# Performance work log

Measured on AMD Instinct MI355X. Metric: run time of the kernel, lower is better.

## Reference

```python
import jax, jax.numpy as jnp
import numpy as np
from jax import lax

THRESH = 0.8
LENS = 0.4
DECAY = 0.2
LOG_SIG_MIN, LOG_SIG_MAX = -20.0, 2.0
WINS = 15

@jax.custom_vjp
def act_fun(x):
    return (x > THRESH).astype(x.dtype)

def _act_fwd(x):
    return act_fun(x), x

def _act_bwd(x, g):
    return (g * (jnp.abs(x - THRESH) < LENS).astype(g.dtype),)

act_fun.defvjp(_act_fwd, _act_bwd)

B, NIN, HID, NACT = 2048, 512, 1024, 32

def _xavier(key, out_d, in_d):
    lim = jnp.sqrt(6.0 / (in_d + out_d)).astype(jnp.float32)
    return jax.random.uniform(key, (out_d, in_d), jnp.float32, -lim, lim)

def setup_inputs() -> dict:
    key = jax.random.key(0)
    ks = jax.random.split(key, 12)
    inp = {
        'state': jax.random.normal(ks[0], (B, 5, NIN), jnp.float32),
        'w1': _xavier(ks[1], HID, NIN), 'b1': jnp.zeros((HID,), jnp.float32),
        'w2': _xavier(ks[2], HID, NIN), 'b2': jnp.zeros((HID,), jnp.float32),
        'w3': _xavier(ks[3], HID, NIN), 'b3': jnp.zeros((HID,), jnp.float32),
        'wl': _xavier(ks[4], 1, 3), 'bl': jnp.zeros((1,), jnp.float32),
        'w11': _xavier(ks[5], HID, 4 * HID), 'b11': jnp.zeros((HID,), jnp.float32),
        'w12': _xavier(ks[6], HID, HID), 'b12': jnp.zeros((HID,), jnp.float32),
        'w21': _xavier(ks[7], HID, 4 * HID), 'b21': jnp.zeros((HID,), jnp.float32),
        'w22': _xavier(ks[8], HID, HID), 'b22': jnp.zeros((HID,), jnp.float32),
        'wm': _xavier(ks[9], NACT, HID), 'bm': jnp.zeros((NACT,), jnp.float32),
        'ws': _xavier(ks[10], NACT, HID), 'bs': jnp.zeros((NACT,), jnp.float32),
    }
    return inp

def _policy_forward(state, w1, b1, w2, b2, w3, b3, wl, bl,
                    w11, b11, w12, b12, w21, b21, w22, b22, wm, bm, ws, bs):
    batch = state.shape[0]
    hid = w1.shape[0]
    seq = jnp.repeat(state, 3, axis=1)
    mem0 = jnp.zeros((batch, hid, 4), state.dtype)
    sp0 = jnp.zeros((batch, hid, 4), state.dtype)

    def step(carry, x_t):
        mem, spike = carry
        i1 = x_t @ w1.T + b1  # [B, HID]
        i2 = x_t @ w2.T + b2
        i3 = x_t @ w3.T + b3
        inner = jnp.einsum('bck,k->bc', mem[:, :, :3], wl[0]) + bl[0]
        inp_all = jnp.stack([i1, i2, i3, inner], axis=-1)  # [B, HID, 4]
        mem1 = mem * DECAY * (1.0 - spike) + inp_all
        sp1 = act_fun(mem1)
        return (mem1, sp1), sp1

    _, spikes = lax.scan(step, (mem0, sp0), jnp.swapaxes(seq, 0, 1))  # [T,B,HID,4]
    spikes = jnp.transpose(spikes, (1, 0, 2, 3)).reshape(batch, WINS, hid * 4)
    x = jnp.mean(spikes, axis=1)  # [B, 4*HID]

    x1 = jax.nn.relu(x @ w11.T + b11)
    x1 = jax.nn.relu(x1 @ w12.T + b12)
    mean = x1 @ wm.T + bm

    x2 = jax.nn.relu(x @ w21.T + b21)
    x2 = jax.nn.relu(x2 @ w22.T + b22)
    log_std = jnp.clip(x2 @ ws.T + bs, LOG_SIG_MIN, LOG_SIG_MAX)
    return mean, log_std

def reference(state, w1, b1, w2, b2, w3, b3, wl, bl,
              w11, b11, w12, b12, w21, b21, w22, b22, wm, bm, ws, bs):
    return _policy_forward(state, w1, b1, w2, b2, w3, b3, wl, bl,
                           w11, b11, w12, b12, w21, b21, w22, b22, wm, bm, ws, bs)
```

## Files before the change

### kernel.cpp

```cpp
#include <hip/hip_runtime.h>
#include <cstddef>
#include <cstdint>

#define THRESH 0.8f
#define DECAY  0.2f

typedef unsigned short ushort_t;
typedef __attribute__((ext_vector_type(8))) short bf16x8;
typedef __attribute__((ext_vector_type(4))) float f32x4;
typedef __attribute__((ext_vector_type(4))) int i32x4;

__device__ __forceinline__ ushort_t f2bf(float f) {
    union { float f; unsigned u; } v; v.f = f;
    unsigned r = v.u + 0x7FFFu + ((v.u >> 16) & 1u);
    return (ushort_t)(r >> 16);
}
__device__ __forceinline__ float bf2f(ushort_t h) {
    union { unsigned u; float f; } v; v.u = ((unsigned)h) << 16;
    return v.f;
}
__device__ __forceinline__ float blo(unsigned u) {
    union { unsigned x; float f; } v; v.x = u << 16; return v.f;
}
__device__ __forceinline__ float bhi(unsigned u) {
    union { unsigned x; float f; } v; v.x = u & 0xFFFF0000u; return v.f;
}

__device__ __forceinline__ void gload16(const void* g, void* l) {
    __builtin_amdgcn_global_load_lds(
        (const __attribute__((address_space(1))) void*)g,
        (__attribute__((address_space(3))) void*)l,
        16, 0, 0);
}

__global__ __launch_bounds__(512, 2) void cur_gemm_qb(
    const ushort_t* __restrict__ A, const ushort_t* __restrict__ W,
    const float* __restrict__ bias, float* __restrict__ C)
{
    __shared__ ushort_t lds[4][16384];

    const int t = threadIdx.x;
    const int mBase = blockIdx.x * 256;
    const int nBase = blockIdx.y * 256;

    const int lane = t & 63;
    const int wv = t >> 6;
    const int wm = (wv >> 2) * 128;
    const int wn = (wv & 3) * 64;
    const int fr = lane & 15;
    const int fq = lane >> 4;
    const int fsw = (fq ^ ((fr >> 1) & 3)) * 8;

    const int r0 = t >> 2;
    const int sc0 = ((t & 3) ^ ((r0 >> 1) & 3)) * 8;
    const size_t aRow0 = (size_t)(mBase + r0) * 1536 + sc0;
    const size_t aRow1 = (size_t)(mBase + r0 + 128) * 1536 + sc0;
    const size_t wRow0 = (size_t)(nBase + r0) * 1536 + sc0;
    const size_t wRow1 = (size_t)(nBase + r0 + 128) * 1536 + sc0;

    f32x4 acc[8][4];
#pragma unroll
    for (int i = 0; i < 8; i++)
#pragma unroll
        for (int j = 0; j < 4; j++) {
            f32x4 z = {0.f, 0.f, 0.f, 0.f};
            acc[i][j] = z;
        }

#define STAGE(tile)                                                   \
    do {                                                              \
        const int k0_ = (tile) * 32;                                  \
        ushort_t* lb_ = &lds[(tile) & 3][0];                          \
        gload16(&A[aRow0 + k0_], &lb_[t * 8]);                        \
        gload16(&A[aRow1 + k0_], &lb_[4096 + t * 8]);                 \
        gload16(&W[wRow0 + k0_], &lb_[8192 + t * 8]);                 \
        gload16(&W[wRow1 + k0_], &lb_[12288 + t * 8]);                \
    } while (0)

    STAGE(0);
    STAGE(1);

    for (int tt = 0; tt < 48; ++tt) {
        if (tt < 47) {
            asm volatile("s_waitcnt vmcnt(4)" ::: "memory");
        } else {
            asm volatile("s_waitcnt vmcnt(0)" ::: "memory");
        }
        __builtin_amdgcn_s_barrier();
        __builtin_amdgcn_sched_barrier(0);
        if (tt < 46) STAGE(tt + 2);

        const ushort_t* lb = &lds[tt & 3][0];
        bf16x8 af[8], wf[4];
#pragma unroll
        for (int i = 0; i < 8; i++)
            af[i] = *(const bf16x8*)&lb[(wm + i * 16 + fr) * 32 + fsw];
#pragma unroll
        for (int j = 0; j < 4; j++)
            wf[j] = *(const bf16x8*)&lb[8192 + (wn + j * 16 + fr) * 32 + fsw];

        __builtin_amdgcn_s_setprio(1);
#pragma unroll
        for (int i = 0; i < 8; i++)
#pragma unroll
            for (int j = 0; j < 4; j++)
                acc[i][j] = __builtin_amdgcn_mfma_f32_16x16x32_bf16(af[i], wf[j], acc[i][j], 0, 0, 0);
        __builtin_amdgcn_s_setprio(0);
    }
#undef STAGE

#pragma unroll
    for (int j = 0; j < 4; j++) {
        const int col = nBase + wn + j * 16 + fr;
        const float bv = bias[col];
#pragma unroll
        for (int i = 0; i < 8; i++)
#pragma unroll
            for (int r = 0; r < 4; r++) {
                const int row = mBase + wm + i * 16 + fq * 4 + r;
                C[(size_t)row * 3072 + col] = acc[i][j][r] + bv;
            }
    }
}

__global__ __launch_bounds__(256) void mlp1_i8(
    const signed char* __restrict__ A, const signed char* __restrict__ W,
    const float* __restrict__ wsc, const float* __restrict__ bias,
    ushort_t* __restrict__ C)
{
    __shared__ signed char sA[64 * 64];
    __shared__ signed char sW[128 * 64];

    const int t = threadIdx.x;
    const int mBase = blockIdx.x * 64;
    const int nBase = blockIdx.y * 128;

    const int lane = t & 63;
    const int wv = t >> 6;
    const int wn = wv * 32;
    const int fr = lane & 15;
    const int fq = lane >> 4;
    const int fsw = (fq ^ ((fr >> 1) & 3)) * 16;

    const int r0 = t >> 2;
    const int cc = ((t & 3) ^ ((t >> 3) & 3)) * 16;

    i32x4 acc[4][2];
#pragma unroll
    for (int i = 0; i < 4; i++)
#pragma unroll
        for (int j = 0; j < 2; j++) {
            i32x4 z = {0, 0, 0, 0};
            acc[i][j] = z;
        }

    for (int k0 = 0; k0 < 4096; k0 += 64) {
        gload16(&A[(size_t)(mBase + r0) * 4096 + k0 + cc], &sA[t * 16]);
        gload16(&W[(size_t)(nBase + r0) * 4096 + k0 + cc], &sW[t * 16]);
        gload16(&W[(size_t)(nBase + 64 + r0) * 4096 + k0 + cc], &sW[4096 + t * 16]);
        __syncthreads();

        i32x4 af[4], wf[2];
#pragma unroll
        for (int i = 0; i < 4; i++)
            af[i] = *(const i32x4*)&sA[(i * 16 + fr) * 64 + fsw];
#pragma unroll
        for (int j = 0; j < 2; j++)
            wf[j] = *(const i32x4*)&sW[(wn + j * 16 + fr) * 64 + fsw];
#pragma unroll
        for (int i = 0; i < 4; i++)
#pragma unroll
            for (int j = 0; j < 2; j++)
                acc[i][j] = __builtin_amdgcn_mfma_i32_16x16x64_i8(af[i], wf[j], acc[i][j], 0, 0, 0);
        __syncthreads();
    }

#pragma unroll
    for (int j = 0; j < 2; j++) {
        const int col = nBase + wn + j * 16 + fr;
        const float sc = wsc[col];
        const float bv = bias[col];
#pragma unroll
        for (int i = 0; i < 4; i++)
#pragma unroll
            for (int r = 0; r < 4; r++) {
                const int row = mBase + i * 16 + fq * 4 + r;
                const float v = (float)acc[i][j][r] * sc + bv;
                C[(size_t)row * 2048 + col] = f2bf(fmaxf(v, 0.f));
            }
    }
}

__global__ __launch_bounds__(256) void mlp2_bf16(
    const ushort_t* __restrict__ A, const ushort_t* __restrict__ W,
    const float* __restrict__ bias, ushort_t* __restrict__ C,
    int N, int K, int lda, int ldw, int ldc, int aHalfOff)
{
    __shared__ ushort_t sA[64 * 32];
    __shared__ ushort_t sW[128 * 32];

    const int t = threadIdx.x;
    const int mBase = blockIdx.x * 64;
    const int nBase = blockIdx.y * 128;
    const int aOff = (2 * nBase >= N) ? aHalfOff : 0;

    const int lane = t & 63;
    const int wv = t >> 6;
    const int wn = wv * 32;
    const int fr = lane & 15;
    const int fq = lane >> 4;
    const int fsw = (fq ^ ((fr >> 1) & 3)) * 8;

    const int r0 = t >> 2;
    const int cc = ((t & 3) ^ ((t >> 3) & 3)) * 8;

    f32x4 acc[4][2];
#pragma unroll
    for (int i = 0; i < 4; i++)
#pragma unroll
        for (int j = 0; j < 2; j++) {
            f32x4 z = {0.f, 0.f, 0.f, 0.f};
            acc[i][j] = z;
        }

    for (int k0 = 0; k0 < K; k0 += 32) {
        gload16(&A[(size_t)(mBase + r0) * lda + aOff + k0 + cc], &sA[t * 8]);
        gload16(&W[(size_t)(nBase + r0) * ldw + k0 + cc], &sW[t * 8]);
        gload16(&W[(size_t)(nBase + 64 + r0) * ldw + k0 + cc], &sW[2048 + t * 8]);
        __syncthreads();

        bf16x8 af[4], wf[2];
#pragma unroll
        for (int i = 0; i < 4; i++)
            af[i] = *(const bf16x8*)&sA[(i * 16 + fr) * 32 + fsw];
#pragma unroll
        for (int j = 0; j < 2; j++)
            wf[j] = *(const bf16x8*)&sW[(wn + j * 16 + fr) * 32 + fsw];
#pragma unroll
        for (int i = 0; i < 4; i++)
#pragma unroll
            for (int j = 0; j < 2; j++)
                acc[i][j] = __builtin_amdgcn_mfma_f32_16x16x32_bf16(af[i], wf[j], acc[i][j], 0, 0, 0);
        __syncthreads();
    }

#pragma unroll
    for (int j = 0; j < 2; j++) {
        const int col = nBase + wn + j * 16 + fr;
        const float bv = bias[col];
#pragma unroll
        for (int i = 0; i < 4; i++)
#pragma unroll
            for (int r = 0; r < 4; r++) {
                const int row = mBase + i * 16 + fq * 4 + r;
                C[(size_t)row * ldc + col] = f2bf(fmaxf(acc[i][j][r] + bv, 0.f));
            }
    }
}

__global__ __launch_bounds__(256) void recur_kernel(
    const float* __restrict__ cur, const float* __restrict__ wl,
    const float* __restrict__ bl, signed char* __restrict__ x)
{
    const int idx = blockIdx.x * 256 + threadIdx.x;
    const int b = idx >> 10, c = idx & 1023;
    const float wl0 = wl[0], wl1 = wl[1], wl2 = wl[2], bl0 = bl[0];
    float m0 = 0, m1 = 0, m2 = 0, m3 = 0;
    int s0 = 0, s1 = 0, s2 = 0, s3 = 0;
#pragma unroll
    for (int f = 0; f < 5; f++) {
        const float* p = cur + (size_t)(b * 5 + f) * 3072 + c;
        const float i1 = p[0], i2 = p[1024], i3 = p[2048];
#pragma unroll
        for (int rep = 0; rep < 3; rep++) {
            const float inner = m0 * wl0 + m1 * wl1 + m2 * wl2 + bl0;
            const float n0 = i1 + ((m0 > THRESH) ? 0.f : DECAY * m0);
            const float n1 = i2 + ((m1 > THRESH) ? 0.f : DECAY * m1);
            const float n2 = i3 + ((m2 > THRESH) ? 0.f : DECAY * m2);
            const float n3 = inner + ((m3 > THRESH) ? 0.f : DECAY * m3);
            m0 = n0; m1 = n1; m2 = n2; m3 = n3;
            s0 += (n0 > THRESH); s1 += (n1 > THRESH);
            s2 += (n2 > THRESH); s3 += (n3 > THRESH);
        }
    }
    uchar4 o;
    o.x = (unsigned char)s0; o.y = (unsigned char)s1;
    o.z = (unsigned char)s2; o.w = (unsigned char)s3;
    *(uchar4*)&x[(size_t)b * 4096 + c * 4] = o;
}

__device__ __forceinline__ void split_state(const float4* src, ushort4* dst,
                                            int base, int t) {
#pragma unroll
    for (int p = 0; p < 4; p++) {
        const int i = base * 1024 + p * 256 + t;
        const float4 v = src[i];
        ushort4 h, l;
        h.x = f2bf(v.x); l.x = f2bf(v.x - bf2f(h.x));
        h.y = f2bf(v.y); l.y = f2bf(v.y - bf2f(h.y));
        h.z = f2bf(v.z); l.z = f2bf(v.z - bf2f(h.z));
        h.w = f2bf(v.w); l.w = f2bf(v.w - bf2f(h.w));
        const int r = i >> 7, c = i & 127;
        ushort4* row = dst + (size_t)r * 384;
        row[c] = h; row[128 + c] = h; row[256 + c] = l;
    }
}
__device__ __forceinline__ void split_w(const float4* src, ushort4* dst,
                                        int base, int t, int roff) {
#pragma unroll
    for (int p = 0; p < 4; p++) {
        const int i = base * 1024 + p * 256 + t;
        const float4 v = src[i];
        ushort4 h, l;
        h.x = f2bf(v.x); l.x = f2bf(v.x - bf2f(h.x));
        h.y = f2bf(v.y); l.y = f2bf(v.y - bf2f(h.y));
        h.z = f2bf(v.z); l.z = f2bf(v.z - bf2f(h.z));
        h.w = f2bf(v.w); l.w = f2bf(v.w - bf2f(h.w));
        const int r = (i >> 7) + roff, c = i & 127;
        ushort4* row = dst + (size_t)r * 384;
        row[c] = h; row[128 + c] = l; row[256 + c] = h;
    }
}
__device__ __forceinline__ void do_cvt4(const float4* src, ushort4* dst,
                                        int base, int t) {
#pragma unroll
    for (int p = 0; p < 4; p++) {
        const int i = base * 1024 + p * 256 + t;
        const float4 v = src[i];
        ushort4 h;
        h.x = f2bf(v.x); h.y = f2bf(v.y); h.z = f2bf(v.z); h.w = f2bf(v.w);
        dst[i] = h;
    }
}
__device__ __forceinline__ int q8(float x, float inv) {
    int q = (int)rintf(x * inv);
    q = q > 127 ? 127 : (q < -127 ? -127 : q);
    return q & 0xff;
}

__global__ __launch_bounds__(256) void prep_kernel(
    const float* __restrict__ state,
    const float* __restrict__ w1, const float* __restrict__ w2,
    const float* __restrict__ w3,
    const float* __restrict__ w11, const float* __restrict__ w21,
    const float* __restrict__ w12, const float* __restrict__ w22,
    const float* __restrict__ b1, const float* __restrict__ b2,
    const float* __restrict__ b3, const float* __restrict__ b11,
    const float* __restrict__ b21, const float* __restrict__ b12,
    const float* __restrict__ b22,
    ushort_t* __restrict__ Ap, ushort_t* __restrict__ Wp,
    signed char* __restrict__ w1q, float* __restrict__ wsc,
    ushort_t* __restrict__ w2b,
    float* __restrict__ b123, float* __restrict__ bb1, float* __restrict__ bb2)
{
    const int bid = blockIdx.x;
    const int t = threadIdx.x;
    if (bid < 1280) {
        split_state((const float4*)state, (ushort4*)Ap, bid, t);
    } else if (bid < 1408) {
        split_w((const float4*)w1, (ushort4*)Wp, bid - 1280, t, 0);
    } else if (bid < 1536) {
        split_w((const float4*)w2, (ushort4*)Wp, bid - 1408, t, 1024);
    } else if (bid < 1664) {
        split_w((const float4*)w3, (ushort4*)Wp, bid - 1536, t, 2048);
    } else if (bid < 3712) {
        const int r = bid - 1664;
        const float* src = (r < 1024) ? (w11 + (size_t)r * 4096)
                                      : (w21 + (size_t)(r - 1024) * 4096);
        __shared__ float red[256];
        float4 v[4];
        float lmax = 0.f;
#pragma unroll
        for (int p = 0; p < 4; p++) {
            v[p] = ((const float4*)src)[t * 4 + p];
            lmax = fmaxf(lmax, fmaxf(fmaxf(fabsf(v[p].x), fabsf(v[p].y)),
                                     fmaxf(fabsf(v[p].z), fabsf(v[p].w))));
        }
        red[t] = lmax;
        __syncthreads();
        for (int s = 128; s > 0; s >>= 1) {
            if (t < s) red[t] = fmaxf(red[t], red[t + s]);
            __syncthreads();
        }
        const float gmax = fmaxf(red[0], 1e-30f);
        const float inv = 127.0f / gmax;
        int4 o;
        o.x = q8(v[0].x, inv) | (q8(v[0].y, inv) << 8) | (q8(v[0].z, inv) << 16) | (q8(v[0].w, inv) << 24);
        o.y = q8(v[1].x, inv) | (q8(v[1].y, inv) << 8) | (q8(v[1].z, inv) << 16) | (q8(v[1].w, inv) << 24);
        o.z = q8(v[2].x, inv) | (q8(v[2].y, inv) << 8) | (q8(v[2].z, inv) << 16) | (q8(v[2].w, inv) << 24);
        o.w = q8(v[3].x, inv) | (q8(v[3].y, inv) << 8) | (q8(v[3].z, inv) << 16) | (q8(v[3].w, inv) << 24);
        ((int4*)(w1q + (size_t)r * 4096))[t] = o;
        if (t == 0) wsc[r] = gmax / (127.0f * 15.0f);
    } else if (bid < 3968) {
        do_cvt4((const float4*)w12, (ushort4*)w2b, bid - 3712, t);
    } else if (bid < 4224) {
        do_cvt4((const float4*)w22, (ushort4*)(w2b + 1048576), bid - 3968, t);
    } else {
#pragma unroll
        for (int p = 0; p < 4; p++) {
            const int i = p * 256 + t;
            b123[i] = b1[i]; b123[1024 + i] = b2[i]; b123[2048 + i] = b3[i];
            bb1[i] = b11[i]; bb1[1024 + i] = b21[i];
            bb2[i] = b12[i]; bb2[1024 + i] = b22[i];
        }
    }
}

__global__ __launch_bounds__(256) void head_kernel(
    const ushort_t* __restrict__ h, const float* __restrict__ wm,
    const float* __restrict__ bm, const float* __restrict__ ws,
    const float* __restrict__ bs, float* __restrict__ out)
{
    const int t = threadIdx.x;
    const int branch = blockIdx.x >> 8;
    const int n = t & 31;
    const int b = (blockIdx.x & 255) * 8 + (t >> 5);
    const ushort_t* hr = h + (size_t)b * 2048 + branch * 1024;
    const float* wr = (branch ? ws : wm) + (size_t)n * 1024;
    float s = 0.f;
#pragma unroll 4
    for (int k = 0; k < 1024; k += 8) {
        const uint4 hv = *(const uint4*)&hr[k];
        const float4 w0 = *(const float4*)&wr[k];
        const float4 w1 = *(const float4*)&wr[k + 4];
        s += blo(hv.x) * w0.x + bhi(hv.x) * w0.y
           + blo(hv.y) * w0.z + bhi(hv.y) * w0.w
           + blo(hv.z) * w1.x + bhi(hv.z) * w1.y
           + blo(hv.w) * w1.z + bhi(hv.w) * w1.w;
    }
    s += (branch ? bs : bm)[n];
    if (branch) s = fminf(fmaxf(s, -20.f), 2.f);
    out[(size_t)branch * 65536 + (size_t)b * 32 + n] = s;
}

extern "C" void kernel_launch(void* const* d_in, const int* in_sizes, int n_in,
                              void* d_out, int out_size, void* d_ws, size_t ws_size,
                              hipStream_t stream)
{
    const float* state = (const float*)d_in[0];
    const float* w1  = (const float*)d_in[1];  const float* b1  = (const float*)d_in[2];
    const float* w2  = (const float*)d_in[3];  const float* b2  = (const float*)d_in[4];
    const float* w3  = (const float*)d_in[5];  const float* b3  = (const float*)d_in[6];
    const float* wl  = (const float*)d_in[7];  const float* bl  = (const float*)d_in[8];
    const float* w11 = (const float*)d_in[9];  const float* b11 = (const float*)d_in[10];
    const float* w12 = (const float*)d_in[11]; const float* b12 = (const float*)d_in[12];
    const float* w21 = (const float*)d_in[13]; const float* b21 = (const float*)d_in[14];
    const float* w22 = (const float*)d_in[15]; const float* b22 = (const float*)d_in[16];
    const float* wm  = (const float*)d_in[17]; const float* bm  = (const float*)d_in[18];
    const float* ws  = (const float*)d_in[19]; const float* bs  = (const float*)d_in[20];
    float* out = (float*)d_out;

    char* wp = (char*)d_ws;
    float*       cur   = (float*)wp;       wp += (size_t)10240 * 3072 * 4;
    ushort_t*    Ap    = (ushort_t*)wp;    wp += (size_t)10240 * 1536 * 2;
    ushort_t*    Wp    = (ushort_t*)wp;    wp += (size_t)3072 * 1536 * 2;
    signed char* xb    = (signed char*)wp; wp += (size_t)2048 * 4096;
    signed char* w1q   = (signed char*)wp; wp += (size_t)2048 * 4096;
    ushort_t*    w2b   = (ushort_t*)wp;    wp += (size_t)2048 * 1024 * 2;
    ushort_t*    h1    = (ushort_t*)wp;    wp += (size_t)2048 * 2048 * 2;
    ushort_t*    h2    = (ushort_t*)wp;    wp += (size_t)2048 * 2048 * 2;
    float*       wsc   = (float*)wp;       wp += 2048 * 4;
    float*       b123  = (float*)wp;       wp += 3072 * 4;
    float*       bb1   = (float*)wp;       wp += 2048 * 4;
    float*       bb2   = (float*)wp;       wp += 2048 * 4;

    prep_kernel<<<4225, 256, 0, stream>>>(
        state, w1, w2, w3, w11, w21, w12, w22,
        b1, b2, b3, b11, b21, b12, b22,
        Ap, Wp, w1q, wsc, w2b, b123, bb1, bb2);

    cur_gemm_qb<<<dim3(40, 12), 512, 0, stream>>>(Ap, Wp, b123, cur);

    recur_kernel<<<8192, 256, 0, stream>>>(cur, wl, bl, xb);

    mlp1_i8<<<dim3(32, 16), 256, 0, stream>>>(xb, w1q, wsc, bb1, h1);

    mlp2_bf16<<<dim3(32, 16), 256, 0, stream>>>(
        h1, w2b, bb2, h2, 2048, 1024, 2048, 1024, 2048, 1024);

    head_kernel<<<512, 256, 0, stream>>>(h2, wm, bm, ws, bs, out);
}
```

Measured before the change: 379.1 us.

## Split GEMM k-step into two phases interleaving LDS reads, global prefetch and MFMA

Result: no change. 386.5 us (+1.9%).

```diff
diff --git a/kernel.cpp b/kernel.cpp
--- a/kernel.cpp
+++ b/kernel.cpp
@@ -33,7 +33,13 @@
         16, 0, 0);
 }
 
-__global__ __launch_bounds__(512, 2) void cur_gemm_qb(
+#define DSREAD(dst, addr, off) \
+    asm volatile("ds_read_b128 %0, %1 offset:" #off : "=v"(dst) : "v"(addr))
+
+#define MM(i, j, a, w) \
+    acc[i][j] = __builtin_amdgcn_mfma_f32_16x16x32_bf16(a, w, acc[i][j], 0, 0, 0)
+
+__global__ __launch_bounds__(512, 2) void cur_gemm_8ph(
     const ushort_t* __restrict__ A, const ushort_t* __restrict__ W,
     const float* __restrict__ bias, float* __restrict__ C)
 {
@@ -49,7 +55,10 @@
     const int wn = (wv & 3) * 64;
     const int fr = lane & 15;
     const int fq = lane >> 4;
-    const int fsw = (fq ^ ((fr >> 1) & 3)) * 8;
+    const int fsw2 = (fq ^ ((fr >> 1) & 3)) * 16;
+
+    const unsigned aBase = (unsigned)((wm + fr) * 64 + fsw2);
+    const unsigned bBase = (unsigned)(16384 + (wn + fr) * 64 + fsw2);
 
     const int r0 = t >> 2;
     const int sc0 = ((t & 3) ^ ((r0 >> 1) & 3)) * 8;
@@ -67,47 +76,67 @@
             acc[i][j] = z;
         }
 
-#define STAGE(tile)                                                   \
-    do {                                                              \
-        const int k0_ = (tile) * 32;                                  \
-        ushort_t* lb_ = &lds[(tile) & 3][0];                          \
-        gload16(&A[aRow0 + k0_], &lb_[t * 8]);                        \
-        gload16(&A[aRow1 + k0_], &lb_[4096 + t * 8]);                 \
-        gload16(&W[wRow0 + k0_], &lb_[8192 + t * 8]);                 \
-        gload16(&W[wRow1 + k0_], &lb_[12288 + t * 8]);                \
-    } while (0)
-
-    STAGE(0);
-    STAGE(1);
+#define STG_A0(tile) gload16(&A[aRow0 + (size_t)(tile) * 32], &lds[(tile) & 3][t * 8])
+#define STG_A1(tile) gload16(&A[aRow1 + (size_t)(tile) * 32], &lds[(tile) & 3][4096 + t * 8])
+#define STG_B0(tile) gload16(&W[wRow0 + (size_t)(tile) * 32], &lds[(tile) & 3][8192 + t * 8])
+#define STG_B1(tile) gload16(&W[wRow1 + (size_t)(tile) * 32], &lds[(tile) & 3][12288 + t * 8])
+
+    STG_A0(0); STG_A1(0); STG_B0(0); STG_B1(0);
+    STG_A0(1); STG_A1(1); STG_B0(1); STG_B1(1);
+    asm volatile("s_waitcnt vmcnt(4)");
+    __builtin_amdgcn_s_barrier();
 
     for (int tt = 0; tt < 48; ++tt) {
-        if (tt < 47) {
-            asm volatile("s_waitcnt vmcnt(4)" ::: "memory");
-        } else {
-            asm volatile("s_waitcnt vmcnt(0)" ::: "memory");
-        }
+        const unsigned bufOff = (unsigned)((tt & 3) << 15);
+        const unsigned av = aBase + bufOff;
+        const unsigned bv = bBase + bufOff;
+        bf16x8 af0, af1, af2, af3, wf0, wf1, wf2, wf3;
+
+        DSREAD(af0, av, 0);
+        DSREAD(af1, av, 1024);
+        DSREAD(af2, av, 2048);
+        DSREAD(af3, av, 3072);
+        DSREAD(wf0, bv, 0);
+        DSREAD(wf1, bv, 1024);
+        DSREAD(wf2, bv, 2048);
+        DSREAD(wf3, bv, 3072);
+        if (tt < 46) { STG_A0(tt + 2); STG_A1(tt + 2); }
         __builtin_amdgcn_s_barrier();
+        asm volatile("s_waitcnt lgkmcnt(0)");
         __builtin_amdgcn_sched_barrier(0);
-        if (tt < 46) STAGE(tt + 2);
-
-        const ushort_t* lb = &lds[tt & 3][0];
-        bf16x8 af[8], wf[4];
-#pragma unroll
-        for (int i = 0; i < 8; i++)
-            af[i] = *(const bf16x8*)&lb[(wm + i * 16 + fr) * 32 + fsw];
-#pragma unroll
-        for (int j = 0; j < 4; j++)
-            wf[j] = *(const bf16x8*)&lb[8192 + (wn + j * 16 + fr) * 32 + fsw];
-
         __builtin_amdgcn_s_setprio(1);
-#pragma unroll
-        for (int i = 0; i < 8; i++)
-#pragma unroll
-            for (int j = 0; j < 4; j++)
-                acc[i][j] = __builtin_amdgcn_mfma_f32_16x16x32_bf16(af[i], wf[j], acc[i][j], 0, 0, 0);
+        MM(0, 0, af0, wf0); MM(0, 1, af0, wf1); MM(0, 2, af0, wf2); MM(0, 3, af0, wf3);
+        MM(1, 0, af1, wf0); MM(1, 1, af1, wf1); MM(1, 2, af1, wf2); MM(1, 3, af1, wf3);
+        MM(2, 0, af2, wf0); MM(2, 1, af2, wf1); MM(2, 2, af2, wf2); MM(2, 3, af2, wf3);
+        MM(3, 0, af3, wf0); MM(3, 1, af3, wf1); MM(3, 2, af3, wf2); MM(3, 3, af3, wf3);
         __builtin_amdgcn_s_setprio(0);
-    }
-#undef STAGE
+        __builtin_amdgcn_s_barrier();
+
+        DSREAD(af0, av, 4096);
+        DSREAD(af1, av, 5120);
+        DSREAD(af2, av, 6144);
+        DSREAD(af3, av, 7168);
+        if (tt < 46) { STG_B0(tt + 2); STG_B1(tt + 2); }
+        if (tt < 46) {
+            asm volatile("s_waitcnt vmcnt(4)");
+        } else if (tt == 46) {
+            asm volatile("s_waitcnt vmcnt(0)");
+        }
+        __builtin_amdgcn_s_barrier();
+        asm volatile("s_waitcnt lgkmcnt(0)");
+        __builtin_amdgcn_sched_barrier(0);
+        __builtin_amdgcn_s_setprio(1);
+        MM(4, 0, af0, wf0); MM(4, 1, af0, wf1); MM(4, 2, af0, wf2); MM(4, 3, af0, wf3);
+        MM(5, 0, af1, wf0); MM(5, 1, af1, wf1); MM(5, 2, af1, wf2); MM(5, 3, af1, wf3);
+        MM(6, 0, af2, wf0); MM(6, 1, af2, wf1); MM(6, 2, af2, wf2); MM(6, 3, af2, wf3);
+        MM(7, 0, af3, wf0); MM(7, 1, af3, wf1); MM(7, 2, af3, wf2); MM(7, 3, af3, wf3);
+        __builtin_amdgcn_s_setprio(0);
+        __builtin_amdgcn_s_barrier();
+    }
+#undef STG_A0
+#undef STG_A1
+#undef STG_B0
+#undef STG_B1
 
 #pragma unroll
     for (int j = 0; j < 4; j++) {
@@ -469,7 +498,7 @@
         b1, b2, b3, b11, b21, b12, b22,
         Ap, Wp, w1q, wsc, w2b, b123, bb1, bb2);
 
-    cur_gemm_qb<<<dim3(40, 12), 512, 0, stream>>>(Ap, Wp, b123, cur);
+    cur_gemm_8ph<<<dim3(40, 12), 512, 0, stream>>>(Ap, Wp, b123, cur);
 
     recur_kernel<<<8192, 256, 0, stream>>>(cur, wl, bl, xb);
 
```

## Fuse input-current GEMM with LIF recurrence via permuted operand layouts

Applied to the files above, without the earlier changes.

New measurement: 370.1 us. 2.4% less time.

```diff
diff --git a/kernel.cpp b/kernel.cpp
--- a/kernel.cpp
+++ b/kernel.cpp
@@ -33,93 +33,158 @@
         16, 0, 0);
 }
 
-__global__ __launch_bounds__(512, 2) void cur_gemm_qb(
+#define DSREAD(dst, addr, off) \
+    asm volatile("ds_read_b128 %0, %1 offset:" #off : "=v"(dst) : "v"(addr))
+
+#define MM(i, j, a, w) \
+    acc[i][j] = __builtin_amdgcn_mfma_f32_16x16x32_bf16(a, w, acc[i][j], 0, 0, 0)
+
+__global__ __launch_bounds__(512, 4) void fused_cur_lif(
     const ushort_t* __restrict__ A, const ushort_t* __restrict__ W,
-    const float* __restrict__ bias, float* __restrict__ C)
+    const float* __restrict__ b123, const float* __restrict__ wl,
+    const float* __restrict__ bl, signed char* __restrict__ xb)
 {
-    __shared__ ushort_t lds[4][16384];
+    __shared__ ushort_t lds[3][11264];
 
     const int t = threadIdx.x;
-    const int mBase = blockIdx.x * 256;
-    const int nBase = blockIdx.y * 256;
-
+    const int bx = blockIdx.x;
+    const int by = blockIdx.y;
     const int lane = t & 63;
     const int wv = t >> 6;
-    const int wm = (wv >> 2) * 128;
-    const int wn = (wv & 3) * 64;
+    const int wm = (wv >> 2) * 80;
+    const int wn = (wv & 3) * 48;
     const int fr = lane & 15;
     const int fq = lane >> 4;
-    const int fsw = (fq ^ ((fr >> 1) & 3)) * 8;
-
-    const int r0 = t >> 2;
-    const int sc0 = ((t & 3) ^ ((r0 >> 1) & 3)) * 8;
-    const size_t aRow0 = (size_t)(mBase + r0) * 1536 + sc0;
-    const size_t aRow1 = (size_t)(mBase + r0 + 128) * 1536 + sc0;
-    const size_t wRow0 = (size_t)(nBase + r0) * 1536 + sc0;
-    const size_t wRow1 = (size_t)(nBase + r0 + 128) * 1536 + sc0;
-
-    f32x4 acc[8][4];
-#pragma unroll
-    for (int i = 0; i < 8; i++)
-#pragma unroll
-        for (int j = 0; j < 4; j++) {
+    const int swz16 = (fq ^ ((fr >> 1) & 3)) * 16;
+
+    const unsigned a0 = (unsigned)((wm + fr) * 64 + swz16);
+    const unsigned b0 = (unsigned)(10240 + (wn + fr) * 64 + swz16);
+
+    const ushort_t* src0; const ushort_t* src1;
+    const ushort_t* src2; const ushort_t* src3;
+    int dst0, dst1, dst2, dst3;
+    if (wv < 5) {
+        const int rl0 = wv * 32 + (lane >> 2);
+        const int rl1 = rl0 + 16;
+        src0 = A + (size_t)(bx * 160 + rl0) * 1536 + ((lane & 3) ^ ((rl0 >> 1) & 3)) * 8;
+        src1 = A + (size_t)(bx * 160 + rl1) * 1536 + ((lane & 3) ^ ((rl1 >> 1) & 3)) * 8;
+        src2 = src0; src3 = src1;
+        dst0 = rl0 * 32 + (lane & 3) * 8;
+        dst1 = rl1 * 32 + (lane & 3) * 8;
+        dst2 = dst0; dst3 = dst1;
+    } else {
+        const int rb = (wv - 5) * 64 + (lane >> 2);
+        src0 = W + (size_t)(by * 192 + rb) * 1536 + ((lane & 3) ^ ((rb >> 1) & 3)) * 8;
+        src1 = src0 + (size_t)16 * 1536;
+        src2 = src0 + (size_t)32 * 1536;
+        src3 = src0 + (size_t)48 * 1536;
+        dst0 = 5120 + rb * 32 + (lane & 3) * 8;
+        dst1 = dst0 + 16 * 32;
+        dst2 = dst0 + 32 * 32;
+        dst3 = dst0 + 48 * 32;
+    }
+
+#define STAGE(tile, sbuf)                                              \
+    do {                                                               \
+        const int k0_ = (tile) * 32;                                   \
+        ushort_t* lb_ = &lds[sbuf][0];                                 \
+        if (wv < 5) {                                                  \
+            gload16(src0 + k0_, lb_ + dst0);                           \
+            gload16(src1 + k0_, lb_ + dst1);                           \
+        } else {                                                       \
+            gload16(src0 + k0_, lb_ + dst0);                           \
+            gload16(src1 + k0_, lb_ + dst1);                           \
+            gload16(src2 + k0_, lb_ + dst2);                           \
+            gload16(src3 + k0_, lb_ + dst3);                           \
+        }                                                              \
+    } while (0)
+
+    f32x4 acc[5][3];
+#pragma unroll
+    for (int i = 0; i < 5; i++)
+#pragma unroll
+        for (int j = 0; j < 3; j++) {
             f32x4 z = {0.f, 0.f, 0.f, 0.f};
             acc[i][j] = z;
         }
 
-#define STAGE(tile)                                                   \
-    do {                                                              \
-        const int k0_ = (tile) * 32;                                  \
-        ushort_t* lb_ = &lds[(tile) & 3][0];                          \
-        gload16(&A[aRow0 + k0_], &lb_[t * 8]);                        \
-        gload16(&A[aRow1 + k0_], &lb_[4096 + t * 8]);                 \
-        gload16(&W[wRow0 + k0_], &lb_[8192 + t * 8]);                 \
-        gload16(&W[wRow1 + k0_], &lb_[12288 + t * 8]);                \
-    } while (0)
-
-    STAGE(0);
-    STAGE(1);
-
+    STAGE(0, 0);
+    STAGE(1, 1);
+
+    int cb = 0, sb = 2;
     for (int tt = 0; tt < 48; ++tt) {
-        if (tt < 47) {
-            asm volatile("s_waitcnt vmcnt(4)" ::: "memory");
+        if (tt < 46) STAGE(tt + 2, sb);
+        if (wv < 5) {
+            if (tt < 46)       asm volatile("s_waitcnt vmcnt(4)" ::: "memory");
+            else if (tt == 46) asm volatile("s_waitcnt vmcnt(2)" ::: "memory");
+            else               asm volatile("s_waitcnt vmcnt(0)" ::: "memory");
         } else {
-            asm volatile("s_waitcnt vmcnt(0)" ::: "memory");
+            if (tt < 46)       asm volatile("s_waitcnt vmcnt(8)" ::: "memory");
+            else if (tt == 46) asm volatile("s_waitcnt vmcnt(4)" ::: "memory");
+            else               asm volatile("s_waitcnt vmcnt(0)" ::: "memory");
         }
         __builtin_amdgcn_s_barrier();
         __builtin_amdgcn_sched_barrier(0);
-        if (tt < 46) STAGE(tt + 2);
-
-        const ushort_t* lb = &lds[tt & 3][0];
-        bf16x8 af[8], wf[4];
-#pragma unroll
-        for (int i = 0; i < 8; i++)
-            af[i] = *(const bf16x8*)&lb[(wm + i * 16 + fr) * 32 + fsw];
-#pragma unroll
-        for (int j = 0; j < 4; j++)
-            wf[j] = *(const bf16x8*)&lb[8192 + (wn + j * 16 + fr) * 32 + fsw];
-
+
+        const unsigned av = (unsigned)(cb * 22528) + a0;
+        const unsigned bv = (unsigned)(cb * 22528) + b0;
+        bf16x8 af0, af1, af2, af3, af4, wf0, wf1, wf2;
+        DSREAD(af0, av, 0);
+        DSREAD(af1, av, 1024);
+        DSREAD(af2, av, 2048);
+        DSREAD(af3, av, 3072);
+        DSREAD(af4, av, 4096);
+        DSREAD(wf0, bv, 0);
+        DSREAD(wf1, bv, 1024);
+        DSREAD(wf2, bv, 2048);
+        asm volatile("s_waitcnt lgkmcnt(0)" ::: "memory");
+        __builtin_amdgcn_sched_barrier(0);
         __builtin_amdgcn_s_setprio(1);
-#pragma unroll
-        for (int i = 0; i < 8; i++)
-#pragma unroll
-            for (int j = 0; j < 4; j++)
-                acc[i][j] = __builtin_amdgcn_mfma_f32_16x16x32_bf16(af[i], wf[j], acc[i][j], 0, 0, 0);
+        MM(0, 0, af0, wf0); MM(0, 1, af0, wf1); MM(0, 2, af0, wf2);
+        MM(1, 0, af1, wf0); MM(1, 1, af1, wf1); MM(1, 2, af1, wf2);
+        MM(2, 0, af2, wf0); MM(2, 1, af2, wf1); MM(2, 2, af2, wf2);
+        MM(3, 0, af3, wf0); MM(3, 1, af3, wf1); MM(3, 2, af3, wf2);
+        MM(4, 0, af4, wf0); MM(4, 1, af4, wf1); MM(4, 2, af4, wf2);
         __builtin_amdgcn_s_setprio(0);
+        __builtin_amdgcn_s_barrier();
+        __builtin_amdgcn_sched_barrier(0);
+
+        cb = (cb == 2) ? 0 : cb + 1;
+        sb = (sb == 2) ? 0 : sb + 1;
     }
 #undef STAGE
 
-#pragma unroll
-    for (int j = 0; j < 4; j++) {
-        const int col = nBase + wn + j * 16 + fr;
-        const float bv = bias[col];
-#pragma unroll
-        for (int i = 0; i < 8; i++)
-#pragma unroll
-            for (int r = 0; r < 4; r++) {
-                const int row = mBase + wm + i * 16 + fq * 4 + r;
-                C[(size_t)row * 3072 + col] = acc[i][j][r] + bv;
+    const int ch = by * 64 + (wv & 3) * 16 + fr;
+    const float b1c = b123[ch];
+    const float b2c = b123[1024 + ch];
+    const float b3c = b123[2048 + ch];
+    const float wl0 = wl[0], wl1 = wl[1], wl2 = wl[2], bl0 = bl[0];
+    const int bbase = bx * 32 + (wv >> 2) * 16 + fq * 4;
+#pragma unroll
+    for (int r = 0; r < 4; r++) {
+        float m0 = 0.f, m1 = 0.f, m2 = 0.f, m3 = 0.f;
+        int s0 = 0, s1 = 0, s2 = 0, s3 = 0;
+#pragma unroll
+        for (int f = 0; f < 5; f++) {
+            const float i1 = acc[f][0][r] + b1c;
+            const float i2 = acc[f][1][r] + b2c;
+            const float i3 = acc[f][2][r] + b3c;
+#pragma unroll
+            for (int rep = 0; rep < 3; rep++) {
+                const float inner = m0 * wl0 + m1 * wl1 + m2 * wl2 + bl0;
+                const float n0 = i1 + ((m0 > THRESH) ? 0.f : DECAY * m0);
+                const float n1 = i2 + ((m1 > THRESH) ? 0.f : DECAY * m1);
+                const float n2 = i3 + ((m2 > THRESH) ? 0.f : DECAY * m2);
+                const float n3 = inner + ((m3 > THRESH) ? 0.f : DECAY * m3);
+                m0 = n0; m1 = n1; m2 = n2; m3 = n3;
+                s0 += (n0 > THRESH); s1 += (n1 > THRESH);
+                s2 += (n2 > THRESH); s3 += (n3 > THRESH);
             }
+        }
+        uchar4 o;
+        o.x = (unsigned char)s0; o.y = (unsigned char)s1;
+        o.z = (unsigned char)s2; o.w = (unsigned char)s3;
+        *(uchar4*)&xb[(size_t)(bbase + r) * 4096 + ch * 4] = o;
     }
 }
 
@@ -258,39 +323,8 @@
     }
 }
 
-__global__ __launch_bounds__(256) void recur_kernel(
-    const float* __restrict__ cur, const float* __restrict__ wl,
-    const float* __restrict__ bl, signed char* __restrict__ x)
-{
-    const int idx = blockIdx.x * 256 + threadIdx.x;
-    const int b = idx >> 10, c = idx & 1023;
-    const float wl0 = wl[0], wl1 = wl[1], wl2 = wl[2], bl0 = bl[0];
-    float m0 = 0, m1 = 0, m2 = 0, m3 = 0;
-    int s0 = 0, s1 = 0, s2 = 0, s3 = 0;
-#pragma unroll
-    for (int f = 0; f < 5; f++) {
-        const float* p = cur + (size_t)(b * 5 + f) * 3072 + c;
-        const float i1 = p[0], i2 = p[1024], i3 = p[2048];
-#pragma unroll
-        for (int rep = 0; rep < 3; rep++) {
-            const float inner = m0 * wl0 + m1 * wl1 + m2 * wl2 + bl0;
-            const float n0 = i1 + ((m0 > THRESH) ? 0.f : DECAY * m0);
-            const float n1 = i2 + ((m1 > THRESH) ? 0.f : DECAY * m1);
-            const float n2 = i3 + ((m2 > THRESH) ? 0.f : DECAY * m2);
-            const float n3 = inner + ((m3 > THRESH) ? 0.f : DECAY * m3);
-            m0 = n0; m1 = n1; m2 = n2; m3 = n3;
-            s0 += (n0 > THRESH); s1 += (n1 > THRESH);
-            s2 += (n2 > THRESH); s3 += (n3 > THRESH);
-        }
-    }
-    uchar4 o;
-    o.x = (unsigned char)s0; o.y = (unsigned char)s1;
-    o.z = (unsigned char)s2; o.w = (unsigned char)s3;
-    *(uchar4*)&x[(size_t)b * 4096 + c * 4] = o;
-}
-
-__device__ __forceinline__ void split_state(const float4* src, ushort4* dst,
-                                            int base, int t) {
+__device__ __forceinline__ void split_state_perm(const float4* src, ushort4* dst,
+                                                 int base, int t) {
 #pragma unroll
     for (int p = 0; p < 4; p++) {
         const int i = base * 1024 + p * 256 + t;
@@ -300,13 +334,15 @@
         h.y = f2bf(v.y); l.y = f2bf(v.y - bf2f(h.y));
         h.z = f2bf(v.z); l.z = f2bf(v.z - bf2f(h.z));
         h.w = f2bf(v.w); l.w = f2bf(v.w - bf2f(h.w));
-        const int r = i >> 7, c = i & 127;
-        ushort4* row = dst + (size_t)r * 384;
-        row[c] = h; row[128 + c] = h; row[256 + c] = l;
-    }
-}
-__device__ __forceinline__ void split_w(const float4* src, ushort4* dst,
-                                        int base, int t, int roff) {
+        const int s = i >> 7, c4 = i & 127;
+        const int b = s / 5, f = s - b * 5;
+        const int m = ((b >> 5) * 160) + (((b >> 4) & 1) * 80) + (f << 4) + (b & 15);
+        ushort4* row = dst + (size_t)m * 384;
+        row[c4] = h; row[128 + c4] = h; row[256 + c4] = l;
+    }
+}
+__device__ __forceinline__ void split_w_perm(const float4* src, ushort4* dst,
+                                             int base, int t, int j) {
 #pragma unroll
     for (int p = 0; p < 4; p++) {
         const int i = base * 1024 + p * 256 + t;
@@ -316,9 +352,10 @@
         h.y = f2bf(v.y); l.y = f2bf(v.y - bf2f(h.y));
         h.z = f2bf(v.z); l.z = f2bf(v.z - bf2f(h.z));
         h.w = f2bf(v.w); l.w = f2bf(v.w - bf2f(h.w));
-        const int r = (i >> 7) + roff, c = i & 127;
-        ushort4* row = dst + (size_t)r * 384;
-        row[c] = h; row[128 + c] = l; row[256 + c] = h;
+        const int c = i >> 7, c4 = i & 127;
+        const int n = ((c >> 6) * 192) + (((c >> 4) & 3) * 48) + (j << 4) + (c & 15);
+        ushort4* row = dst + (size_t)n * 384;
+        row[c4] = h; row[128 + c4] = l; row[256 + c4] = h;
     }
 }
 __device__ __forceinline__ void do_cvt4(const float4* src, ushort4* dst,
@@ -356,13 +393,13 @@
     const int bid = blockIdx.x;
     const int t = threadIdx.x;
     if (bid < 1280) {
-        split_state((const float4*)state, (ushort4*)Ap, bid, t);
+        split_state_perm((const float4*)state, (ushort4*)Ap, bid, t);
     } else if (bid < 1408) {
-        split_w((const float4*)w1, (ushort4*)Wp, bid - 1280, t, 0);
+        split_w_perm((const float4*)w1, (ushort4*)Wp, bid - 1280, t, 0);
     } else if (bid < 1536) {
-        split_w((const float4*)w2, (ushort4*)Wp, bid - 1408, t, 1024);
+        split_w_perm((const float4*)w2, (ushort4*)Wp, bid - 1408, t, 1);
     } else if (bid < 1664) {
-        split_w((const float4*)w3, (ushort4*)Wp, bid - 1536, t, 2048);
+        split_w_perm((const float4*)w3, (ushort4*)Wp, bid - 1536, t, 2);
     } else if (bid < 3712) {
         const int r = bid - 1664;
         const float* src = (r < 1024) ? (w11 + (size_t)r * 4096)
@@ -451,7 +488,6 @@
     float* out = (float*)d_out;
 
     char* wp = (char*)d_ws;
-    float*       cur   = (float*)wp;       wp += (size_t)10240 * 3072 * 4;
     ushort_t*    Ap    = (ushort_t*)wp;    wp += (size_t)10240 * 1536 * 2;
     ushort_t*    Wp    = (ushort_t*)wp;    wp += (size_t)3072 * 1536 * 2;
     signed char* xb    = (signed char*)wp; wp += (size_t)2048 * 4096;
@@ -469,9 +505,7 @@
         b1, b2, b3, b11, b21, b12, b22,
         Ap, Wp, w1q, wsc, w2b, b123, bb1, bb2);
 
-    cur_gemm_qb<<<dim3(40, 12), 512, 0, stream>>>(Ap, Wp, b123, cur);
-
-    recur_kernel<<<8192, 256, 0, stream>>>(cur, wl, bl, xb);
+    fused_cur_lif<<<dim3(64, 16), 512, 0, stream>>>(Ap, Wp, b123, wl, bl, xb);
 
     mlp1_i8<<<dim3(32, 16), 256, 0, stream>>>(xb, w1q, wsc, bb1, h1);
 
```
